# Kernel optimization log

Hardware: AMD Instinct MI355X
Metric: run time of the kernel (lower is better)

Reference implementation:

```python
import jax, jax.numpy as jnp
import numpy as np

BS, QLEN, DIM, NH = 2, 2048, 1024, 16
HD = DIM // NH


def setup_inputs() -> dict:
    key = jax.random.key(0)
    ks = jax.random.split(key, 6)
    std = 0.02
    return {
        "x": jax.random.normal(ks[0], (BS, QLEN, DIM), dtype=jnp.float32),
        "mask": jnp.ones((BS, QLEN), dtype=jnp.float32),
        "Wq": jax.random.normal(ks[1], (DIM, DIM), dtype=jnp.float32) * std,
        "bq": jnp.zeros((DIM,), dtype=jnp.float32),
        "Wk": jax.random.normal(ks[2], (DIM, DIM), dtype=jnp.float32) * std,
        "bk": jnp.zeros((DIM,), dtype=jnp.float32),
        "Wv": jax.random.normal(ks[3], (DIM, DIM), dtype=jnp.float32) * std,
        "bv": jnp.zeros((DIM,), dtype=jnp.float32),
        "Wo": jax.random.normal(ks[4], (DIM, DIM), dtype=jnp.float32) * std,
        "bo": jnp.zeros((DIM,), dtype=jnp.float32),
    }


def reference(x, mask, Wq, bq, Wk, bk, Wv, bv, Wo, bo):
    bs, qlen, dim = x.shape
    # project and split heads: [bs, nh, len, hd]
    def split_heads(t):
        return t.reshape(bs, -1, NH, HD).transpose(0, 2, 1, 3)

    q = split_heads(x @ Wq + bq) / jnp.sqrt(jnp.float32(HD))
    k = split_heads(x @ Wk + bk)
    v = split_heads(x @ Wv + bv)

    scores = jnp.einsum("bhqd,bhkd->bhqk", q, k)  # [bs, nh, qlen, klen]
    m = mask.reshape(bs, 1, 1, -1)  # 2D mask -> broadcast over heads and q
    scores = scores - 1e30 * (1.0 - m)
    weights = jax.nn.softmax(scores, axis=-1)
    # dropout p=0.0 at inference -> no-op; head_mask is None
    context = jnp.einsum("bhqk,bhkd->bhqd", weights, v)
    context = context.transpose(0, 2, 1, 3).reshape(bs, qlen, NH * HD)
    return context @ Wo + bo
```

## Files before the change

kernel.cpp:

```cpp
#include <hip/hip_runtime.h>
#include <stdint.h>

#define BSZ  2
#define SEQ  2048
#define DIM  1024
#define NHD  16
#define HD   64
#define MTOT (BSZ*SEQ)

using short8  = __attribute__((ext_vector_type(8))) short;
using floatx4 = __attribute__((ext_vector_type(4))) float;

#define QSCALE 0.18033688011112042f
#define BIGM   1.44e30f

__device__ __forceinline__ unsigned short f2bf(float f) {
    unsigned int u = __float_as_uint(f);
    u += 0x7fffu + ((u >> 16) & 1u);
    return (unsigned short)(u >> 16);
}
__device__ __forceinline__ unsigned int pk2r(float a, float b) {
    unsigned int ua = __float_as_uint(a) + 0x8000u;
    unsigned int ub = __float_as_uint(b) + 0x8000u;
    return __builtin_amdgcn_perm(ub, ua, 0x07060302);
}
__device__ __forceinline__ unsigned int cvtpk(float a, float b) {
    unsigned int r;
    asm("v_cvt_pk_bf16_f32 %0, %1, %2" : "=v"(r) : "v"(a), "v"(b));
    return r;
}

__device__ __forceinline__ void gll16(const void* g, const void* lds) {
    unsigned int loff = (unsigned int)(unsigned long long)lds;
    __builtin_amdgcn_global_load_lds(
        (const __attribute__((address_space(1))) unsigned int*)g,
        (__attribute__((address_space(3))) unsigned int*)loff, 16, 0, 0);
}

__global__ __launch_bounds__(256)
void conv_x(const float* __restrict__ X, const float* __restrict__ mask,
            unsigned short* __restrict__ Xbf, float* __restrict__ Pen) {
    size_t i = ((size_t)blockIdx.x * 256 + threadIdx.x) * 8;
    float4 a = *(const float4*)(X + i);
    float4 b = *(const float4*)(X + i + 4);
    uint4 u = {pk2r(a.x, a.y), pk2r(a.z, a.w), pk2r(b.x, b.y), pk2r(b.z, b.w)};
    *(uint4*)(Xbf + i) = u;
    if (blockIdx.x < 2) {
        const size_t j = ((size_t)blockIdx.x * 256 + threadIdx.x) * 8;
        float4 m0 = *(const float4*)(mask + j);
        float4 m1 = *(const float4*)(mask + j + 4);
        float4 r0 = {__builtin_fmaf(m0.x, BIGM, -BIGM), __builtin_fmaf(m0.y, BIGM, -BIGM),
                     __builtin_fmaf(m0.z, BIGM, -BIGM), __builtin_fmaf(m0.w, BIGM, -BIGM)};
        float4 r1 = {__builtin_fmaf(m1.x, BIGM, -BIGM), __builtin_fmaf(m1.y, BIGM, -BIGM),
                     __builtin_fmaf(m1.z, BIGM, -BIGM), __builtin_fmaf(m1.w, BIGM, -BIGM)};
        *(float4*)(Pen + j)     = r0;
        *(float4*)(Pen + j + 4) = r1;
    }
}

__global__ __launch_bounds__(256)
void conv_wt(const float* __restrict__ Wq, const float* __restrict__ Wk,
             const float* __restrict__ Wv, const float* __restrict__ Wo,
             unsigned short* __restrict__ Wt3, unsigned short* __restrict__ Wto)
{
    __shared__ float tile[64 * 65];
    const int z = blockIdx.z;
    const float* W = (z == 0) ? Wq : (z == 1) ? Wk : (z == 2) ? Wv : Wo;
    unsigned short* out = (z < 3) ? (Wt3 + (size_t)z * DIM * DIM) : Wto;
    const int k0 = blockIdx.x * 64, n0 = blockIdx.y * 64;
    const int t = threadIdx.x;
    const int r = t >> 2, c0 = (t & 3) * 16;
#pragma unroll
    for (int j = 0; j < 4; ++j) {
        float4 v = *(const float4*)&W[(size_t)(k0 + r) * DIM + n0 + c0 + j * 4];
        tile[r * 65 + c0 + j * 4 + 0] = v.x;
        tile[r * 65 + c0 + j * 4 + 1] = v.y;
        tile[r * 65 + c0 + j * 4 + 2] = v.z;
        tile[r * 65 + c0 + j * 4 + 3] = v.w;
    }
    __syncthreads();
    unsigned int p[8];
#pragma unroll
    for (int j = 0; j < 8; ++j)
        p[j] = pk2r(tile[(c0 + 2 * j) * 65 + r], tile[(c0 + 2 * j + 1) * 65 + r]);
    uint4 u0 = {p[0], p[1], p[2], p[3]}, u1 = {p[4], p[5], p[6], p[7]};
    unsigned short* dst = out + (size_t)(n0 + r) * DIM + k0 + c0;
    *(uint4*)dst = u0;
    *(uint4*)(dst + 8) = u1;
}

__global__ __launch_bounds__(256)
void qkv_gemm(const unsigned short* __restrict__ Xbf,
              const unsigned short* __restrict__ Wt3,
              const float* __restrict__ bq, const float* __restrict__ bk,
              const float* __restrict__ bv,
              unsigned short* __restrict__ Qb,
              unsigned short* __restrict__ Kb,
              unsigned short* __restrict__ VbT)
{
    __shared__ unsigned short As[2][128 * 32];
    __shared__ unsigned short Bs[2][128 * 32];

    const int t = threadIdx.x, w = t >> 6, lane = t & 63;
    const int lm = lane & 15, grp = lane >> 4;
    const int wm = w >> 1, wn = w & 1;
    const int m0 = blockIdx.x * 128;
    const int mat = blockIdx.y >> 3;
    const int n0 = (blockIdx.y & 7) * 128;
    const unsigned short* Bg = Wt3 + (size_t)mat * DIM * DIM;
    const int lr = lane >> 2, lc = (lane & 3) * 8;
    const int r0 = w * 16;
    const bool swap = (mat != 2);

    const unsigned short* xs0 = Xbf + (size_t)(m0 + r0 + lr) * DIM + lc;
    const unsigned short* xs1 = Xbf + (size_t)(m0 + 64 + r0 + lr) * DIM + lc;
    const unsigned short* ws0 = Bg  + (size_t)(n0 + r0 + lr) * DIM + lc;
    const unsigned short* ws1 = Bg  + (size_t)(n0 + 64 + r0 + lr) * DIM + lc;

    const unsigned short* afb[2];
    const unsigned short* bfb[2];
#pragma unroll
    for (int u = 0; u < 2; ++u) {
        afb[u] = &As[u][(wm * 64 + lm) * 32 + grp * 8];
        bfb[u] = &Bs[u][(wn * 64 + lm) * 32 + grp * 8];
    }

    floatx4 acc[4][4];
#pragma unroll
    for (int i = 0; i < 4; ++i)
#pragma unroll
        for (int j = 0; j < 4; ++j) acc[i][j] = (floatx4){0.f, 0.f, 0.f, 0.f};

#define QKV_STAGE(BUF) do {                                    \
        gll16(xs0, &As[BUF][r0 * 32]);                         \
        gll16(xs1, &As[BUF][(64 + r0) * 32]);                  \
        gll16(ws0, &Bs[BUF][r0 * 32]);                         \
        gll16(ws1, &Bs[BUF][(64 + r0) * 32]);                  \
        xs0 += 32; xs1 += 32; ws0 += 32; ws1 += 32;            \
    } while (0)

#define QKV_BODY(CUR) do {                                                    \
        __syncthreads();                                                      \
        QKV_STAGE(CUR ^ 1);                                                   \
        short8 af[4], bf[4];                                                  \
        _Pragma("unroll")                                                     \
        for (int mt = 0; mt < 4; ++mt)                                        \
            af[mt] = *(const short8*)(afb[CUR] + mt * 512);                   \
        _Pragma("unroll")                                                     \
        for (int nt = 0; nt < 4; ++nt)                                        \
            bf[nt] = *(const short8*)(bfb[CUR] + nt * 512);                   \
        if (swap) {                                                           \
            _Pragma("unroll")                                                 \
            for (int mt = 0; mt < 4; ++mt)                                    \
                _Pragma("unroll")                                             \
                for (int nt = 0; nt < 4; ++nt)                                \
                    acc[mt][nt] = __builtin_amdgcn_mfma_f32_16x16x32_bf16(    \
                        bf[nt], af[mt], acc[mt][nt], 0, 0, 0);                \
        } else {                                                              \
            _Pragma("unroll")                                                 \
            for (int mt = 0; mt < 4; ++mt)                                    \
                _Pragma("unroll")                                             \
                for (int nt = 0; nt < 4; ++nt)                                \
                    acc[mt][nt] = __builtin_amdgcn_mfma_f32_16x16x32_bf16(    \
                        af[mt], bf[nt], acc[mt][nt], 0, 0, 0);                \
        }                                                                     \
    } while (0)

    QKV_STAGE(0);
#pragma unroll 1
    for (int it = 0; it < DIM / 64; ++it) {
        QKV_BODY(0);
        QKV_BODY(1);
    }
#undef QKV_BODY
#undef QKV_STAGE

    if (mat == 2) {
#pragma unroll
        for (int nt = 0; nt < 4; ++nt) {
            const int c = n0 + wn * 64 + nt * 16 + lm;
            const float bb = bv[c];
            const int h = c >> 6, d = c & 63;
#pragma unroll
            for (int mt = 0; mt < 4; ++mt) {
                const int r = m0 + wm * 64 + mt * 16 + grp * 4;
                const int b = r >> 11, s = r & 2047;
                const int si = s & 63, sb = s & ~63;
                const int cg = si >> 4, g = (si >> 2) & 3;
                const int unit = (((cg & 1) << 2) | g) ^ (d & 7);
                const int sph = sb + unit * 8 + ((cg >> 1) << 2);
                uint2 pv;
                pv.x = pk2r(acc[mt][nt][0] + bb, acc[mt][nt][1] + bb);
                pv.y = pk2r(acc[mt][nt][2] + bb, acc[mt][nt][3] + bb);
                *(uint2*)&VbT[(((size_t)(b * NHD + h)) * HD + d) * SEQ + sph] = pv;
            }
        }
    } else {
        const float* bias = (mat == 0) ? bq : bk;
        unsigned short* dst = (mat == 0) ? Qb : Kb;
        const float sc = (mat == 0) ? QSCALE : 1.0f;
#pragma unroll
        for (int nt = 0; nt < 4; ++nt) {
            const int c0 = n0 + wn * 64 + nt * 16 + grp * 4;
            float4 bb = *(const float4*)&bias[c0];
            const int h = c0 >> 6, d0 = c0 & 63;
#pragma unroll
            for (int mt = 0; mt < 4; ++mt) {
                const int r = m0 + wm * 64 + mt * 16 + lm;
                const int b = r >> 11, s = r & 2047;
                uint2 pv;
                pv.x = pk2r((acc[mt][nt][0] + bb.x) * sc, (acc[mt][nt][1] + bb.y) * sc);
                pv.y = pk2r((acc[mt][nt][2] + bb.z) * sc, (acc[mt][nt][3] + bb.w) * sc);
                const int dd = (mat == 0) ? d0
                             : ((((d0 >> 3) ^ (s & 7)) << 3) | (d0 & 7));
                *(uint2*)&dst[(((size_t)(b * NHD + h)) * SEQ + s) * HD + dd] = pv;
            }
        }
    }
}

__global__ __launch_bounds__(256, 4)
void attn(const unsigned short* __restrict__ Qb,
          const unsigned short* __restrict__ Kb,
          const unsigned short* __restrict__ VbT,
          const float* __restrict__ Pen,
          unsigned short* __restrict__ Cb)
{
    __shared__ unsigned short Kt[2][64 * 64];
    __shared__ unsigned short Vt[2][64 * 64];

    const int t = threadIdx.x, w = t >> 6, lane = t & 63;
    const int lm = lane & 15, grp = lane >> 4;
    const int x7 = lm & 7;

    const int lin = blockIdx.y * (int)gridDim.x + blockIdx.x;
    const int swz = (lin & 7) * ((SEQ / 64) * (BSZ * NHD) / 8) + (lin >> 3);
    const int bh = swz >> 5, b = bh >> 4, h = bh & 15;
    const int q0 = (swz & 31) * 64;

    short8 qf[2];
    {
        const unsigned short* qrow = Qb + ((size_t)bh * SEQ + q0 + w * 16 + lm) * HD;
        qf[0] = *(const short8*)(qrow + grp * 8);
        qf[1] = *(const short8*)(qrow + 32 + grp * 8);
    }

    const unsigned int one2 = 0x3f803f80u;
    uint4 onesu = {one2, one2, one2, one2};
    short8 ones = *(const short8*)&onesu;

    floatx4 oacc[4];
#pragma unroll
    for (int i = 0; i < 4; ++i) oacc[i] = (floatx4){0.f, 0.f, 0.f, 0.f};
    floatx4 lacc = (floatx4){0.f, 0.f, 0.f, 0.f};

    const unsigned short* Kg = Kb + (size_t)bh * SEQ * HD;
    const unsigned short* Vg = VbT + (size_t)bh * HD * SEQ;
    const int srow = lane >> 3, scol = (lane & 7) * 8;

    const unsigned short* kp0 = Kg + (size_t)(w * 16 + srow) * HD + scol;
    const unsigned short* kp1 = kp0 + 8 * HD;
    const unsigned short* vp0 = Vg + (size_t)(w * 16 + srow) * SEQ + scol;
    const unsigned short* vp1 = vp0 + 8 * SEQ;

    gll16(kp0, &Kt[0][(w * 16) * 64]);
    gll16(kp1, &Kt[0][(w * 16 + 8) * 64]);
    gll16(vp0, &Vt[0][(w * 16) * 64]);
    gll16(vp1, &Vt[0][(w * 16 + 8) * 64]);
    kp0 += 64 * HD; kp1 += 64 * HD; vp0 += 64; vp1 += 64;

    const unsigned short* kba[2]; const unsigned short* kbb[2];
    const unsigned short* vba[2]; const unsigned short* vbb[2];
#pragma unroll
    for (int u = 0; u < 2; ++u) {
        kba[u] = &Kt[u][lm * 64 + ((grp    ) ^ x7) * 8];
        kbb[u] = &Kt[u][lm * 64 + ((4 + grp) ^ x7) * 8];
        vba[u] = &Vt[u][lm * 64 + ((grp    ) ^ x7) * 8];
        vbb[u] = &Vt[u][lm * 64 + ((4 + grp) ^ x7) * 8];
    }
    const float* mp = Pen + (size_t)b * SEQ + grp * 4;

#define ATTN_BODY(CUR) do {                                                   \
        __syncthreads();                                                      \
        gll16(kp0, &Kt[CUR ^ 1][(w * 16) * 64]);                              \
        gll16(kp1, &Kt[CUR ^ 1][(w * 16 + 8) * 64]);                          \
        gll16(vp0, &Vt[CUR ^ 1][(w * 16) * 64]);                              \
        gll16(vp1, &Vt[CUR ^ 1][(w * 16 + 8) * 64]);                          \
        kp0 += 64 * HD; kp1 += 64 * HD; vp0 += 64; vp1 += 64;                 \
        float4 mdv[4];                                                        \
        _Pragma("unroll")                                                     \
        for (int cg = 0; cg < 4; ++cg)                                        \
            mdv[cg] = *(const float4*)(mp + cg * 16);                         \
        mp += 64;                                                             \
        floatx4 sv[4];                                                        \
        __builtin_amdgcn_s_setprio(1);                                        \
        _Pragma("unroll")                                                     \
        for (int cg = 0; cg < 4; ++cg) {                                      \
            short8 a0 = *(const short8*)(kba[CUR] + cg * 1024);               \
            short8 a1 = *(const short8*)(kbb[CUR] + cg * 1024);               \
            floatx4 s = (floatx4){mdv[cg].x, mdv[cg].y, mdv[cg].z, mdv[cg].w}; \
            s = __builtin_amdgcn_mfma_f32_16x16x32_bf16(a0, qf[0], s, 0, 0, 0); \
            s = __builtin_amdgcn_mfma_f32_16x16x32_bf16(a1, qf[1], s, 0, 0, 0); \
            sv[cg] = s;                                                       \
        }                                                                     \
        __builtin_amdgcn_s_setprio(0);                                        \
        short8 vf[4][2];                                                      \
        _Pragma("unroll")                                                     \
        for (int dg = 0; dg < 4; ++dg) {                                      \
            vf[dg][0] = *(const short8*)(vba[CUR] + dg * 1024);               \
            vf[dg][1] = *(const short8*)(vbb[CUR] + dg * 1024);               \
        }                                                                     \
        float p[4][4];                                                        \
        _Pragma("unroll")                                                     \
        for (int cg = 0; cg < 4; ++cg) {                                      \
            p[cg][0] = __builtin_exp2f(sv[cg][0]);                            \
            p[cg][1] = __builtin_exp2f(sv[cg][1]);                            \
            p[cg][2] = __builtin_exp2f(sv[cg][2]);                            \
            p[cg][3] = __builtin_exp2f(sv[cg][3]);                            \
        }                                                                     \
        uint4 u0, u1;                                                         \
        u0.x = cvtpk(p[0][0], p[0][1]); u0.y = cvtpk(p[0][2], p[0][3]);       \
        u0.z = cvtpk(p[2][0], p[2][1]); u0.w = cvtpk(p[2][2], p[2][3]);       \
        u1.x = cvtpk(p[1][0], p[1][1]); u1.y = cvtpk(p[1][2], p[1][3]);       \
        u1.z = cvtpk(p[3][0], p[3][1]); u1.w = cvtpk(p[3][2], p[3][3]);       \
        short8 ap0 = *(const short8*)&u0;                                     \
        short8 ap1 = *(const short8*)&u1;                                     \
        __builtin_amdgcn_s_setprio(1);                                        \
        _Pragma("unroll")                                                     \
        for (int dg = 0; dg < 4; ++dg) {                                      \
            oacc[dg] = __builtin_amdgcn_mfma_f32_16x16x32_bf16(ap0, vf[dg][0], oacc[dg], 0, 0, 0); \
            oacc[dg] = __builtin_amdgcn_mfma_f32_16x16x32_bf16(ap1, vf[dg][1], oacc[dg], 0, 0, 0); \
        }                                                                     \
        lacc = __builtin_amdgcn_mfma_f32_16x16x32_bf16(ap0, ones, lacc, 0, 0, 0); \
        lacc = __builtin_amdgcn_mfma_f32_16x16x32_bf16(ap1, ones, lacc, 0, 0, 0); \
        __builtin_amdgcn_s_setprio(0);                                        \
    } while (0)

#pragma unroll 1
    for (int it = 0; it < SEQ / 128; ++it) {
        ATTN_BODY(0);
        ATTN_BODY(1);
    }
#undef ATTN_BODY

    float inv[4];
#pragma unroll
    for (int r = 0; r < 4; ++r) inv[r] = (lacc[r] > 0.f) ? 1.0f / lacc[r] : 0.f;
#pragma unroll
    for (int dg = 0; dg < 4; ++dg)
#pragma unroll
        for (int r = 0; r < 4; ++r) {
            const int s = q0 + w * 16 + grp * 4 + r;
            Cb[((size_t)(b * SEQ + s)) * DIM + h * HD + dg * 16 + lm] =
                f2bf(oacc[dg][r] * inv[r]);
        }
}

__global__ __launch_bounds__(256)
void out_gemm(const unsigned short* __restrict__ Cb,
              const unsigned short* __restrict__ Wto,
              const float* __restrict__ bo,
              float* __restrict__ out)
{
    __shared__ unsigned short As[2][128 * 32];
    __shared__ unsigned short Bs[2][64 * 32];

    const int t = threadIdx.x, w = t >> 6, lane = t & 63;
    const int lm = lane & 15, grp = lane >> 4;
    const int m0 = blockIdx.x * 128;
    const int n0 = blockIdx.y * 64;
    const int lr = lane >> 2, lc = (lane & 3) * 8;
    const int r0 = w * 16;

    const unsigned short* cs0 = Cb  + (size_t)(m0 + r0 + lr) * DIM + lc;
    const unsigned short* cs1 = Cb  + (size_t)(m0 + 64 + r0 + lr) * DIM + lc;
    const unsigned short* ws0 = Wto + (size_t)(n0 + r0 + lr) * DIM + lc;

    const unsigned short* afb[2];
    const unsigned short* bfb[2];
#pragma unroll
    for (int u = 0; u < 2; ++u) {
        afb[u] = &As[u][(w * 32 + lm) * 32 + grp * 8];
        bfb[u] = &Bs[u][lm * 32 + grp * 8];
    }

    floatx4 acc[2][4];
#pragma unroll
    for (int i = 0; i < 2; ++i)
#pragma unroll
        for (int j = 0; j < 4; ++j) acc[i][j] = (floatx4){0.f, 0.f, 0.f, 0.f};

#define OUT_STAGE(BUF) do {                                    \
        gll16(cs0, &As[BUF][r0 * 32]);                         \
        gll16(cs1, &As[BUF][(64 + r0) * 32]);                  \
        gll16(ws0, &Bs[BUF][r0 * 32]);                         \
        cs0 += 32; cs1 += 32; ws0 += 32;                       \
    } while (0)

#define OUT_BODY(CUR) do {                                                    \
        __syncthreads();                                                      \
        OUT_STAGE(CUR ^ 1);                                                   \
        short8 af[2], bf[4];                                                  \
        _Pragma("unroll")                                                     \
        for (int mt = 0; mt < 2; ++mt)                                        \
            af[mt] = *(const short8*)(afb[CUR] + mt * 512);                   \
        _Pragma("unroll")                                                     \
        for (int nt = 0; nt < 4; ++nt)                                        \
            bf[nt] = *(const short8*)(bfb[CUR] + nt * 512);                   \
        _Pragma("unroll")                                                     \
        for (int mt = 0; mt < 2; ++mt)                                        \
            _Pragma("unroll")                                                 \
            for (int nt = 0; nt < 4; ++nt)                                    \
                acc[mt][nt] = __builtin_amdgcn_mfma_f32_16x16x32_bf16(        \
                    bf[nt], af[mt], acc[mt][nt], 0, 0, 0);                    \
    } while (0)

    OUT_STAGE(0);
#pragma unroll 1
    for (int it = 0; it < DIM / 64; ++it) {
        OUT_BODY(0);
        OUT_BODY(1);
    }
#undef OUT_BODY
#undef OUT_STAGE

#pragma unroll
    for (int nt = 0; nt < 4; ++nt) {
        const int c0 = n0 + nt * 16 + grp * 4;
        float4 bb = *(const float4*)&bo[c0];
#pragma unroll
        for (int mt = 0; mt < 2; ++mt) {
            const int r = m0 + w * 32 + mt * 16 + lm;
            float4 o = {acc[mt][nt][0] + bb.x, acc[mt][nt][1] + bb.y,
                        acc[mt][nt][2] + bb.z, acc[mt][nt][3] + bb.w};
            *(float4*)&out[(size_t)r * DIM + c0] = o;
        }
    }
}

extern "C" void kernel_launch(void* const* d_in, const int* in_sizes, int n_in,
                              void* d_out, int out_size, void* d_ws, size_t ws_size,
                              hipStream_t stream)
{
    const float* x    = (const float*)d_in[0];
    const float* mask = (const float*)d_in[1];
    const float* Wq   = (const float*)d_in[2];
    const float* bq   = (const float*)d_in[3];
    const float* Wk   = (const float*)d_in[4];
    const float* bk   = (const float*)d_in[5];
    const float* Wv   = (const float*)d_in[6];
    const float* bv   = (const float*)d_in[7];
    const float* Wo   = (const float*)d_in[8];
    const float* bo   = (const float*)d_in[9];
    float* out = (float*)d_out;

    const size_t M1 = (size_t)DIM * DIM;
    unsigned short* Qb  = (unsigned short*)d_ws;
    unsigned short* Kb  = Qb  + 4 * M1;
    unsigned short* VbT = Kb  + 4 * M1;
    unsigned short* Cb  = VbT + 4 * M1;
    unsigned short* Xbf = Cb  + 4 * M1;
    unsigned short* Wt3 = Xbf + 4 * M1;
    unsigned short* Wto = Wt3 + 3 * M1;
    float*          Pen = (float*)(Wto + M1);

    conv_x <<<dim3((MTOT * DIM) / 2048), 256, 0, stream>>>(x, mask, Xbf, Pen);
    conv_wt<<<dim3(16, 16, 4), 256, 0, stream>>>(Wq, Wk, Wv, Wo, Wt3, Wto);
    qkv_gemm<<<dim3(MTOT / 128, 24), 256, 0, stream>>>(Xbf, Wt3, bq, bk, bv, Qb, Kb, VbT);
    attn<<<dim3(SEQ / 64, BSZ * NHD), 256, 0, stream>>>(Qb, Kb, VbT, Pen, Cb);
    out_gemm<<<dim3(MTOT / 128, DIM / 64), 256, 0, stream>>>(Cb, Wto, bo, out);
}
```

Before: 201.7 us.

## Triple-buffer K/V tiles in attention with partial vmcnt waits

The attention kernel moves from double to triple buffering of K and V tiles in shared memory, prefetching two tiles ahead. It replaces the full __syncthreads with a partial s_waitcnt vmcnt(4) plus a raw barrier, so the next tile's loads stay in flight while the current one is consumed. This aims to hide global-load latency better. In exchange it uses more LDS per block and lowers the launch-bounds occupancy hint from 4 to 3 blocks per CU. The loop runs 32 tiles as ten unrolled groups of three plus two trailing bodies; the last iterations prefetch past the end of the per-head K/V range.

After: 215.3 us. 1.07x slower.

```diff
diff --git a/kernel.cpp b/kernel.cpp
--- a/kernel.cpp
+++ b/kernel.cpp
@@ -219,15 +219,15 @@
     }
 }
 
-__global__ __launch_bounds__(256, 4)
+__global__ __launch_bounds__(256, 3)
 void attn(const unsigned short* __restrict__ Qb,
           const unsigned short* __restrict__ Kb,
           const unsigned short* __restrict__ VbT,
           const float* __restrict__ Pen,
           unsigned short* __restrict__ Cb)
 {
-    __shared__ unsigned short Kt[2][64 * 64];
-    __shared__ unsigned short Vt[2][64 * 64];
+    __shared__ unsigned short Kt[3][64 * 64];
+    __shared__ unsigned short Vt[3][64 * 64];
 
     const int t = threadIdx.x, w = t >> 6, lane = t & 63;
     const int lm = lane & 15, grp = lane >> 4;
@@ -247,7 +247,7 @@
 
     const unsigned int one2 = 0x3f803f80u;
     uint4 onesu = {one2, one2, one2, one2};
-    short8 ones = *(const short8*)&onesu;
+    const short8 ones = *(const short8*)&onesu;
 
     floatx4 oacc[4];
 #pragma unroll
@@ -263,16 +263,19 @@
     const unsigned short* vp0 = Vg + (size_t)(w * 16 + srow) * SEQ + scol;
     const unsigned short* vp1 = vp0 + 8 * SEQ;
 
-    gll16(kp0, &Kt[0][(w * 16) * 64]);
-    gll16(kp1, &Kt[0][(w * 16 + 8) * 64]);
-    gll16(vp0, &Vt[0][(w * 16) * 64]);
-    gll16(vp1, &Vt[0][(w * 16 + 8) * 64]);
-    kp0 += 64 * HD; kp1 += 64 * HD; vp0 += 64; vp1 += 64;
-
-    const unsigned short* kba[2]; const unsigned short* kbb[2];
-    const unsigned short* vba[2]; const unsigned short* vbb[2];
-#pragma unroll
-    for (int u = 0; u < 2; ++u) {
+#pragma unroll
+    for (int pb = 0; pb < 2; ++pb) {
+        gll16(kp0, &Kt[pb][(w * 16) * 64]);
+        gll16(kp1, &Kt[pb][(w * 16 + 8) * 64]);
+        gll16(vp0, &Vt[pb][(w * 16) * 64]);
+        gll16(vp1, &Vt[pb][(w * 16 + 8) * 64]);
+        kp0 += 64 * HD; kp1 += 64 * HD; vp0 += 64; vp1 += 64;
+    }
+
+    const unsigned short* kba[3]; const unsigned short* kbb[3];
+    const unsigned short* vba[3]; const unsigned short* vbb[3];
+#pragma unroll
+    for (int u = 0; u < 3; ++u) {
         kba[u] = &Kt[u][lm * 64 + ((grp    ) ^ x7) * 8];
         kbb[u] = &Kt[u][lm * 64 + ((4 + grp) ^ x7) * 8];
         vba[u] = &Vt[u][lm * 64 + ((grp    ) ^ x7) * 8];
@@ -280,24 +283,27 @@
     }
     const float* mp = Pen + (size_t)b * SEQ + grp * 4;
 
-#define ATTN_BODY(CUR) do {                                                   \
-        __syncthreads();                                                      \
-        gll16(kp0, &Kt[CUR ^ 1][(w * 16) * 64]);                              \
-        gll16(kp1, &Kt[CUR ^ 1][(w * 16 + 8) * 64]);                          \
-        gll16(vp0, &Vt[CUR ^ 1][(w * 16) * 64]);                              \
-        gll16(vp1, &Vt[CUR ^ 1][(w * 16 + 8) * 64]);                          \
-        kp0 += 64 * HD; kp1 += 64 * HD; vp0 += 64; vp1 += 64;                 \
+#define ATTN_BODY(RD, WR) do {                                                \
+        asm volatile("s_waitcnt vmcnt(4)" ::: "memory");                      \
+        __builtin_amdgcn_s_barrier();                                         \
+        asm volatile("" ::: "memory");                                        \
         float4 mdv[4];                                                        \
         _Pragma("unroll")                                                     \
         for (int cg = 0; cg < 4; ++cg)                                        \
             mdv[cg] = *(const float4*)(mp + cg * 16);                         \
         mp += 64;                                                             \
+        __builtin_amdgcn_sched_barrier(0);                                    \
+        gll16(kp0, &Kt[WR][(w * 16) * 64]);                                   \
+        gll16(kp1, &Kt[WR][(w * 16 + 8) * 64]);                               \
+        gll16(vp0, &Vt[WR][(w * 16) * 64]);                                   \
+        gll16(vp1, &Vt[WR][(w * 16 + 8) * 64]);                               \
+        kp0 += 64 * HD; kp1 += 64 * HD; vp0 += 64; vp1 += 64;                 \
         floatx4 sv[4];                                                        \
         __builtin_amdgcn_s_setprio(1);                                        \
         _Pragma("unroll")                                                     \
         for (int cg = 0; cg < 4; ++cg) {                                      \
-            short8 a0 = *(const short8*)(kba[CUR] + cg * 1024);               \
-            short8 a1 = *(const short8*)(kbb[CUR] + cg * 1024);               \
+            short8 a0 = *(const short8*)(kba[RD] + cg * 1024);                \
+            short8 a1 = *(const short8*)(kbb[RD] + cg * 1024);                \
             floatx4 s = (floatx4){mdv[cg].x, mdv[cg].y, mdv[cg].z, mdv[cg].w}; \
             s = __builtin_amdgcn_mfma_f32_16x16x32_bf16(a0, qf[0], s, 0, 0, 0); \
             s = __builtin_amdgcn_mfma_f32_16x16x32_bf16(a1, qf[1], s, 0, 0, 0); \
@@ -307,8 +313,8 @@
         short8 vf[4][2];                                                      \
         _Pragma("unroll")                                                     \
         for (int dg = 0; dg < 4; ++dg) {                                      \
-            vf[dg][0] = *(const short8*)(vba[CUR] + dg * 1024);               \
-            vf[dg][1] = *(const short8*)(vbb[CUR] + dg * 1024);               \
+            vf[dg][0] = *(const short8*)(vba[RD] + dg * 1024);                \
+            vf[dg][1] = *(const short8*)(vbb[RD] + dg * 1024);                \
         }                                                                     \
         float p[4][4];                                                        \
         _Pragma("unroll")                                                     \
@@ -337,11 +343,16 @@
     } while (0)
 
 #pragma unroll 1
-    for (int it = 0; it < SEQ / 128; ++it) {
-        ATTN_BODY(0);
-        ATTN_BODY(1);
-    }
+    for (int it = 0; it < 10; ++it) {
+        ATTN_BODY(0, 2);
+        ATTN_BODY(1, 0);
+        ATTN_BODY(2, 1);
+    }
+    ATTN_BODY(0, 2);
+    ATTN_BODY(1, 0);
 #undef ATTN_BODY
+
+    asm volatile("s_waitcnt vmcnt(0)" ::: "memory");
 
     float inv[4];
 #pragma unroll
```
